# Optimization experiments

Hardware: AMD Instinct MI355X
Metric: run time of the kernel (lower is better)

## Reference

```python
import jax, jax.numpy as jnp
import numpy as np

B, NE, NR, D1, D2, L = 64, 40000, 500, 200, 200, 64
BN_EPS = 1e-5


def _batchnorm(x, gamma, beta):
    # training-mode BatchNorm1d: biased batch statistics over axis 0
    mu = jnp.mean(x, axis=0)
    var = jnp.var(x, axis=0)
    return gamma * (x - mu) * jax.lax.rsqrt(var + BN_EPS) + beta


def setup_inputs() -> dict:
    key = jax.random.key(0)
    ks = jax.random.split(key, 10)
    return {
        "e1_idx": jax.random.randint(ks[0], (B,), 0, NE),
        "r_idx": jax.random.randint(ks[1], (B,), 0, NR),
        "E": jax.random.normal(ks[2], (NE, D1), dtype=jnp.float32),
        "R": jax.random.normal(ks[3], (NR, D2), dtype=jnp.float32),
        # W ~ Uniform(-1, 1) as in the torch module
        "W": jax.random.uniform(ks[4], (D2, D1, D1), dtype=jnp.float32, minval=-1.0, maxval=1.0),
        # literals normalized into [0, 1]
        "lits": jax.random.uniform(ks[5], (NE, L), dtype=jnp.float32),
        "c": jax.random.normal(ks[6], (L,), dtype=jnp.float32) * 0.1,
        # variance buffer must be positive
        "var_l": jax.random.uniform(ks[7], (L,), dtype=jnp.float32, minval=0.5, maxval=1.5),
        "nf": jax.random.normal(ks[8], (NR, L), dtype=jnp.float32) * 0.1,
        "bn0_gamma": jnp.ones((D1,), jnp.float32),
        "bn0_beta": jnp.zeros((D1,), jnp.float32),
        "bn1_gamma": jnp.ones((D1,), jnp.float32),
        "bn1_beta": jnp.zeros((D1,), jnp.float32),
    }


def reference(e1_idx, r_idx, E, R, W, lits, c, var_l, nf,
              bn0_gamma, bn0_beta, bn1_gamma, bn1_beta):
    # --- TuckER core ---
    e1 = E[e1_idx]                                   # (B, d1)
    x = _batchnorm(e1, bn0_gamma, bn0_beta)          # (B, d1)
    r = R[r_idx]                                     # (B, d2)
    W_mat = jnp.einsum('bk,kij->bij', r, W)          # (B, d1, d1)
    x = jnp.einsum('bi,bij->bj', x, W_mat)           # (B, d1)
    x = _batchnorm(x, bn1_gamma, bn1_beta)
    score_l = x @ E.T                                # (B, N)

    # --- KBLN numeric-literal branch ---
    n_h = lits[e1_idx]                               # (B, L)
    # broadcast instead of .repeat: (B, 1, L) - (1, N, L) -> (B, N, L)
    n = n_h[:, None, :] - lits[None, :, :]
    phi = jnp.exp(-jnp.square(n - c) / var_l)        # (B, N, L)
    w_nf = nf[r_idx]                                 # (B, L)
    score_n = jnp.einsum('bnl,bl->bn', phi, w_nf)    # (B, N)

    return jax.nn.sigmoid(score_l + score_n)
```

## Files before the change

### kernel.cpp

```cpp
#include <hip/hip_runtime.h>
#include <math.h>

#define BB    64
#define NEC   40000
#define NRC   500
#define D1C   200
#define D2C   200
#define LLC   64
#define BN_EPS 1e-5f
#define LOG2E 1.4426950408889634f

#define WS_XT    0
#define WS_RT    12800
#define WS_TAP   25600
#define WS_WP    29696
#define WS_SL    33792
#define WS_X2BH  33856
#define WS_X2BL  42048
#define WS_Y     50240

typedef short s8v __attribute__((ext_vector_type(8)));
typedef float f4v __attribute__((ext_vector_type(4)));

__device__ __forceinline__ unsigned short bf16_rne(float x) {
  unsigned b = __float_as_uint(x);
  unsigned r = b + 0x7FFFu + ((b >> 16) & 1u);
  return (unsigned short)(r >> 16);
}
__device__ __forceinline__ void split2(float x, unsigned short& h,
                                       unsigned short& l) {
  h = bf16_rne(x);
  float hf = __uint_as_float(((unsigned)h) << 16);
  l = bf16_rne(x - hf);
}

typedef __attribute__((address_space(1))) const void gvoid_t;
typedef __attribute__((address_space(3))) void lvoid_t;
__device__ __forceinline__ void gload_lds16(const float* g, float* l) {
  __builtin_amdgcn_global_load_lds((gvoid_t*)g, (lvoid_t*)l, 16, 0, 0);
}

__global__ __launch_bounds__(256) void prep_kernel(
    const int* __restrict__ e1_idx, const int* __restrict__ r_idx,
    const float* __restrict__ E, const float* __restrict__ R,
    const float* __restrict__ lits, const float* __restrict__ c,
    const float* __restrict__ var_l, const float* __restrict__ nf,
    const float* __restrict__ bn0g, const float* __restrict__ bn0b,
    float* __restrict__ ws) {
  float* xT  = ws + WS_XT;
  float* rT  = ws + WS_RT;
  float* taP = ws + WS_TAP;
  float* wP  = ws + WS_WP;
  float* sl  = ws + WS_SL;
  int tid = threadIdx.x;

  if (blockIdx.x == 0) {
    if (tid < D1C) {
      int j = tid;
      float sum = 0.f, sq = 0.f;
      for (int b = 0; b < BB; b++) {
        float e = E[e1_idx[b] * D1C + j];
        sum += e; sq += e * e;
      }
      float mean = sum * (1.f / 64.f);
      float var  = sq  * (1.f / 64.f) - mean * mean;
      float inv  = __builtin_amdgcn_rsqf(var + BN_EPS);
      float g    = bn0g[j] * inv;
      float be   = bn0b[j] - mean * g;
      for (int b = 0; b < BB; b++) {
        xT[j * 64 + b] = g * E[e1_idx[b] * D1C + j] + be;
      }
    }
  } else if (blockIdx.x == 1) {
    for (int idx = tid; idx < D2C * 64; idx += 256) {
      int k = idx >> 6, b = idx & 63;
      rT[idx] = R[r_idx[b] * D2C + k];
    }
  } else if (blockIdx.x == 2) {
    for (int idx = tid; idx < LLC * 64; idx += 256) {
      int l = idx >> 6, b = idx & 63;
      float s = sqrtf(LOG2E / var_l[l]);
      float a = (lits[e1_idx[b] * LLC + l] - c[l]) * s;
      int bp = (b & 15) * 4 + (b >> 4);
      taP[l * 64 + bp] = a + a;
      wP[l * 64 + bp]  = nf[r_idx[b] * LLC + l] * __builtin_amdgcn_exp2f(-a * a);
    }
    if (tid < LLC) sl[tid] = sqrtf(LOG2E / var_l[tid]);
  } else {
    unsigned* z = (unsigned*)(ws + WS_X2BH);
    for (int i = tid; i < 16384; i += 256) z[i] = 0u;
  }
}

#define S1_STAGE(buf_, s_) do {                                         \
    int gbase_ = kbase + (s_) * 8000;                                   \
    _Pragma("unroll")                                                   \
    for (int r_ = 0; r_ < 4; r_++) {                                    \
      int off_ = r_ * 2048 + w * 256;                                   \
      int gi_ = gbase_ + off_ + lane4;                                  \
      gi_ = gi_ < 7999996 ? gi_ : 7999996;                              \
      gload_lds16(W + gi_, &Wb[buf_][off_]);                            \
    }                                                                   \
  } while (0)

__global__ __launch_bounds__(512) void stage1_kernel(
    const float* __restrict__ W, const float* __restrict__ ws_in,
    float* __restrict__ y) {
  const float* xT = ws_in + WS_XT;
  const float* rT = ws_in + WS_RT;
  __shared__ float Wb[2][8192];

  int k = blockIdx.x;
  int tid = threadIdx.x;
  int lane = tid & 63;
  int w = __builtin_amdgcn_readfirstlane(tid >> 6);
  int jc = w & 3, bh = w >> 2;
  int j4 = lane & 15, bq = lane >> 4;
  int j0 = jc * 64 + j4 * 4;
  int b0 = bh * 32 + bq * 8;
  bool jok = j0 < 200;
  int joff = jok ? j0 : 0;
  int kbase = k * 40000;
  int lane4 = lane * 4;

  float acc[4][8];
#pragma unroll
  for (int jj = 0; jj < 4; jj++)
#pragma unroll
    for (int bb = 0; bb < 8; bb++) acc[jj][bb] = 0.f;

  S1_STAGE(0, 0);
  for (int s = 0; s < 5; s++) {
    __syncthreads();
    if (s < 4) S1_STAGE((s + 1) & 1, s + 1);
    const float* Ws = Wb[s & 1];
    const float* xrow = xT + s * 40 * 64 + b0;
#pragma unroll 4
    for (int ri = 0; ri < 40; ri++) {
      float4 wv  = *(const float4*)(Ws + ri * 200 + joff);
      float4 xa  = *(const float4*)(xrow + ri * 64);
      float4 xb2 = *(const float4*)(xrow + ri * 64 + 4);
      float wc[4] = {wv.x, wv.y, wv.z, wv.w};
      float xv[8] = {xa.x, xa.y, xa.z, xa.w, xb2.x, xb2.y, xb2.z, xb2.w};
#pragma unroll
      for (int jj = 0; jj < 4; jj++)
#pragma unroll
        for (int bb = 0; bb < 8; bb++)
          acc[jj][bb] += wc[jj] * xv[bb];
    }
  }

  if (jok) {
    float4 r0 = *(const float4*)(rT + k * 64 + b0);
    float4 r1 = *(const float4*)(rT + k * 64 + b0 + 4);
    float rv[8] = {r0.x, r0.y, r0.z, r0.w, r1.x, r1.y, r1.z, r1.w};
#pragma unroll
    for (int jj = 0; jj < 4; jj++) {
      float* yo = y + (k * D1C + j0 + jj) * 64 + b0;
      float4 o0 = make_float4(acc[jj][0] * rv[0], acc[jj][1] * rv[1],
                              acc[jj][2] * rv[2], acc[jj][3] * rv[3]);
      float4 o1 = make_float4(acc[jj][4] * rv[4], acc[jj][5] * rv[5],
                              acc[jj][6] * rv[6], acc[jj][7] * rv[7]);
      *(float4*)(yo) = o0;
      *(float4*)(yo + 4) = o1;
    }
  }
}

__global__ __launch_bounds__(256) void reduce_bn1_kernel(
    const float* __restrict__ y, const float* __restrict__ bn1g,
    const float* __restrict__ bn1b, float* __restrict__ ws) {
  int j = blockIdx.x;
  int tid = threadIdx.x, b = tid & 63, kq = tid >> 6;

  float s = 0.f;
  const float* yp = y + (kq * 50 * D1C + j) * 64 + b;
#pragma unroll 10
  for (int k = 0; k < 50; k++) s += yp[k * D1C * 64];

  __shared__ float part[256];
  part[tid] = s;
  __syncthreads();
  if (tid < 64) {
    float v = part[tid] + part[64 + tid] + part[128 + tid] + part[192 + tid];
    float sum = v, sq = v * v;
#pragma unroll
    for (int o = 32; o > 0; o >>= 1) {
      sum += __shfl_xor(sum, o, 64);
      sq  += __shfl_xor(sq,  o, 64);
    }
    float mean = sum * (1.f / 64.f);
    float var  = sq  * (1.f / 64.f) - mean * mean;
    float inv  = __builtin_amdgcn_rsqf(var + BN_EPS);
    float g    = bn1g[j] * inv;
    float be   = bn1b[j] - mean * g;
    float xv   = g * v + be;
    unsigned short h, l;
    split2(xv, h, l);
    unsigned short* xh = (unsigned short*)(ws + WS_X2BH);
    unsigned short* xl = (unsigned short*)(ws + WS_X2BL);
    xh[tid * 256 + j] = h;
    xl[tid * 256 + j] = l;
  }
}

__global__ __launch_bounds__(256, 4) void final_kernel(
    const float* __restrict__ E, const float* __restrict__ lits,
    const float* __restrict__ ws, float* __restrict__ out) {
  const float* taP = ws + WS_TAP;
  const float* wP  = ws + WS_WP;
  const float* sl  = ws + WS_SL;
  const unsigned short* x2bh = (const unsigned short*)(ws + WS_X2BH);
  const unsigned short* x2bl = (const unsigned short*)(ws + WS_X2BL);

  __shared__ float SM[9216];
  unsigned short* Ah = (unsigned short*)SM;
  unsigned short* Al = Ah + 4608;
  unsigned short* Bh = Ah + 9216;
  unsigned short* Bl = Ah + 13824;

  int n0 = blockIdx.x * 64;
  int tid = threadIdx.x;
  int lane = tid & 63;
  int w = __builtin_amdgcn_readfirstlane(tid >> 6);
  int ln = lane & 15;
  int quad = lane >> 4;

  f4v acc[4];
#pragma unroll
  for (int t = 0; t < 4; t++) acc[t] = (f4v){0.f, 0.f, 0.f, 0.f};

  for (int q = 0; q < 4; q++) {
    int k0 = q * 64;
    __syncthreads();
#pragma unroll
    for (int it = 0; it < 4; it++) {
      int idx = tid + it * 256;
      int row = idx >> 4, c4 = idx & 15, cc = c4 * 4;
      float4 v = make_float4(0.f, 0.f, 0.f, 0.f);
      if (k0 + cc < 200) v = *(const float4*)(E + (n0 + row) * D1C + k0 + cc);
      unsigned short h0, l0, h1, l1, h2, l2, h3, l3;
      split2(v.x, h0, l0); split2(v.y, h1, l1);
      split2(v.z, h2, l2); split2(v.w, h3, l3);
      *(ushort4*)(Ah + row * 72 + cc) = make_ushort4(h0, h1, h2, h3);
      *(ushort4*)(Al + row * 72 + cc) = make_ushort4(l0, l1, l2, l3);
    }
#pragma unroll
    for (int it = 0; it < 4; it++) {
      int idx = tid + it * 256;
      int row = idx >> 4, c4 = idx & 15;
      *(ushort4*)(Bh + row * 72 + c4 * 4) =
          *(const ushort4*)(x2bh + row * 256 + k0 + c4 * 4);
      *(ushort4*)(Bl + row * 72 + c4 * 4) =
          *(const ushort4*)(x2bl + row * 256 + k0 + c4 * 4);
    }
    __syncthreads();

    const unsigned short* Ab  = Ah + (16 * w + ln) * 72 + quad * 8;
    const unsigned short* Alb = Al + (16 * w + ln) * 72 + quad * 8;
#pragma unroll
    for (int ks = 0; ks < 64; ks += 32) {
      s8v ah = *(const s8v*)(Ab + ks);
      s8v al = *(const s8v*)(Alb + ks);
#pragma unroll
      for (int t = 0; t < 4; t++) {
        s8v bh = *(const s8v*)(Bh + (16 * t + ln) * 72 + quad * 8 + ks);
        s8v bl = *(const s8v*)(Bl + (16 * t + ln) * 72 + quad * 8 + ks);
        acc[t] = __builtin_amdgcn_mfma_f32_16x16x32_bf16(ah, bh, acc[t], 0, 0, 0);
        acc[t] = __builtin_amdgcn_mfma_f32_16x16x32_bf16(al, bh, acc[t], 0, 0, 0);
        acc[t] = __builtin_amdgcn_mfma_f32_16x16x32_bf16(ah, bl, acc[t], 0, 0, 0);
      }
    }
  }

  float* Llds = SM;
  float* TAl  = SM + 4352;
  float* Wl   = SM + 6400;
  int nlb = 16 * w + 4 * quad;

  __syncthreads();
#pragma unroll
  for (int it = 0; it < 4; it++) {
    int idx = tid + it * 256;
    int row = idx >> 4, c4 = idx & 15;
    float4 v = *(const float4*)(lits + (n0 + row) * LLC + c4 * 4);
    int l = c4 * 4;
    Llds[(l + 0) * 68 + row] = v.x * sl[l + 0];
    Llds[(l + 1) * 68 + row] = v.y * sl[l + 1];
    Llds[(l + 2) * 68 + row] = v.z * sl[l + 2];
    Llds[(l + 3) * 68 + row] = v.w * sl[l + 3];
  }

  for (int h = 0; h < 2; h++) {
    __syncthreads();
#pragma unroll
    for (int it = 0; it < 2; it++) {
      int idx = tid + it * 256;
      ((float4*)TAl)[idx] = ((const float4*)(taP + h * 2048))[idx];
      ((float4*)Wl)[idx]  = ((const float4*)(wP  + h * 2048))[idx];
    }
    __syncthreads();
    for (int ll = 0; ll < 32; ll++) {
      float4 Lv = *(const float4*)(Llds + (h * 32 + ll) * 68 + nlb);
      float4 ta = *(const float4*)(TAl + ll * 64 + 4 * ln);
      float4 wv = *(const float4*)(Wl  + ll * 64 + 4 * ln);
      float Lc[4]  = {Lv.x, Lv.y, Lv.z, Lv.w};
      float tac[4] = {ta.x, ta.y, ta.z, ta.w};
      float wvc[4] = {wv.x, wv.y, wv.z, wv.w};
      float n2[4];
#pragma unroll
      for (int r = 0; r < 4; r++) n2[r] = -Lc[r] * Lc[r];
#pragma unroll
      for (int t = 0; t < 4; t++) {
#pragma unroll
        for (int r = 0; r < 4; r++) {
          acc[t][r] += wvc[t] *
              __builtin_amdgcn_exp2f(__builtin_fmaf(tac[t], Lc[r], n2[r]));
        }
      }
    }
  }

#pragma unroll
  for (int t = 0; t < 4; t++) {
    float4 o;
    o.x = __builtin_amdgcn_rcpf(1.f + __builtin_amdgcn_exp2f(-LOG2E * acc[t][0]));
    o.y = __builtin_amdgcn_rcpf(1.f + __builtin_amdgcn_exp2f(-LOG2E * acc[t][1]));
    o.z = __builtin_amdgcn_rcpf(1.f + __builtin_amdgcn_exp2f(-LOG2E * acc[t][2]));
    o.w = __builtin_amdgcn_rcpf(1.f + __builtin_amdgcn_exp2f(-LOG2E * acc[t][3]));
    *(float4*)(out + (size_t)(16 * t + ln) * NEC + n0 + nlb) = o;
  }
}

extern "C" void kernel_launch(void* const* d_in, const int* in_sizes, int n_in,
                              void* d_out, int out_size, void* d_ws, size_t ws_size,
                              hipStream_t stream) {
  (void)in_sizes; (void)n_in; (void)out_size; (void)ws_size;
  const int*   e1    = (const int*)d_in[0];
  const int*   ri    = (const int*)d_in[1];
  const float* E     = (const float*)d_in[2];
  const float* R     = (const float*)d_in[3];
  const float* W     = (const float*)d_in[4];
  const float* lits  = (const float*)d_in[5];
  const float* c     = (const float*)d_in[6];
  const float* var_l = (const float*)d_in[7];
  const float* nf    = (const float*)d_in[8];
  const float* bn0g  = (const float*)d_in[9];
  const float* bn0b  = (const float*)d_in[10];
  const float* bn1g  = (const float*)d_in[11];
  const float* bn1b  = (const float*)d_in[12];
  float* out = (float*)d_out;
  float* ws  = (float*)d_ws;
  float* y   = ws + WS_Y;

  prep_kernel<<<4, 256, 0, stream>>>(e1, ri, E, R, lits, c, var_l, nf,
                                     bn0g, bn0b, ws);
  stage1_kernel<<<200, 512, 0, stream>>>(W, ws, y);
  reduce_bn1_kernel<<<200, 256, 0, stream>>>(y, bn1g, bn1b, ws);
  final_kernel<<<625, 256, 0, stream>>>(E, lits, ws, out);
}
```

Measured before the change: 202.9 us.

## Split final kernel into MFMA score kernel and literal-branch kernel

The fused final kernel is split in two. One kernel computes the TuckER matmul scores with MFMA and writes the raw logits to the output. A second kernel, launched on a 2D grid that splits the batch rows in half, reads those logits back, adds the exp-heavy literal score, and applies the sigmoid. The aim is more parallelism and less register pressure for the exp-bound part, at the cost of an extra round trip of the 64x40000 output through memory and one more launch.

```diff
diff --git a/kernel.cpp b/kernel.cpp
--- a/kernel.cpp
+++ b/kernel.cpp
@@ -204,12 +204,9 @@
   }
 }
 
-__global__ __launch_bounds__(256, 4) void final_kernel(
-    const float* __restrict__ E, const float* __restrict__ lits,
-    const float* __restrict__ ws, float* __restrict__ out) {
-  const float* taP = ws + WS_TAP;
-  const float* wP  = ws + WS_WP;
-  const float* sl  = ws + WS_SL;
+__global__ __launch_bounds__(256) void final_l_kernel(
+    const float* __restrict__ E, const float* __restrict__ ws,
+    float* __restrict__ out) {
   const unsigned short* x2bh = (const unsigned short*)(ws + WS_X2BH);
   const unsigned short* x2bl = (const unsigned short*)(ws + WS_X2BL);
 
@@ -273,12 +270,31 @@
     }
   }
 
-  float* Llds = SM;
-  float* TAl  = SM + 4352;
-  float* Wl   = SM + 6400;
   int nlb = 16 * w + 4 * quad;
-
-  __syncthreads();
+#pragma unroll
+  for (int t = 0; t < 4; t++) {
+    *(f4v*)(out + (size_t)(16 * t + ln) * NEC + n0 + nlb) = acc[t];
+  }
+}
+
+__global__ __launch_bounds__(256) void final_n_kernel(
+    const float* __restrict__ lits, const float* __restrict__ ws,
+    float* __restrict__ out) {
+  const float* taP = ws + WS_TAP;
+  const float* wP  = ws + WS_WP;
+  const float* sl  = ws + WS_SL;
+
+  __shared__ float Llds[64 * 68];
+
+  int n0 = blockIdx.x * 64;
+  int yb = blockIdx.y;
+  int tid = threadIdx.x;
+  int lane = tid & 63;
+  int w = __builtin_amdgcn_readfirstlane(tid >> 6);
+  int ln = lane & 15;
+  int quad = lane >> 4;
+  int nlb = 16 * w + 4 * quad;
+
 #pragma unroll
   for (int it = 0; it < 4; it++) {
     int idx = tid + it * 256;
@@ -291,43 +307,44 @@
     Llds[(l + 3) * 68 + row] = v.w * sl[l + 3];
   }
 
-  for (int h = 0; h < 2; h++) {
-    __syncthreads();
-#pragma unroll
-    for (int it = 0; it < 2; it++) {
-      int idx = tid + it * 256;
-      ((float4*)TAl)[idx] = ((const float4*)(taP + h * 2048))[idx];
-      ((float4*)Wl)[idx]  = ((const float4*)(wP  + h * 2048))[idx];
-    }
-    __syncthreads();
-    for (int ll = 0; ll < 32; ll++) {
-      float4 Lv = *(const float4*)(Llds + (h * 32 + ll) * 68 + nlb);
-      float4 ta = *(const float4*)(TAl + ll * 64 + 4 * ln);
-      float4 wv = *(const float4*)(Wl  + ll * 64 + 4 * ln);
-      float Lc[4]  = {Lv.x, Lv.y, Lv.z, Lv.w};
-      float tac[4] = {ta.x, ta.y, ta.z, ta.w};
-      float wvc[4] = {wv.x, wv.y, wv.z, wv.w};
-      float n2[4];
-#pragma unroll
-      for (int r = 0; r < 4; r++) n2[r] = -Lc[r] * Lc[r];
-#pragma unroll
-      for (int t = 0; t < 4; t++) {
-#pragma unroll
-        for (int r = 0; r < 4; r++) {
-          acc[t][r] += wvc[t] *
-              __builtin_amdgcn_exp2f(__builtin_fmaf(tac[t], Lc[r], n2[r]));
-        }
+  f4v acc[2];
+#pragma unroll
+  for (int tt = 0; tt < 2; tt++) {
+    int t = 2 * yb + tt;
+    acc[tt] = *(const f4v*)(out + (size_t)(16 * t + ln) * NEC + n0 + nlb);
+  }
+  __syncthreads();
+
+  int tw = 4 * ln + 2 * yb;
+#pragma unroll 2
+  for (int ll = 0; ll < 64; ll++) {
+    float4 Lv = *(const float4*)(&Llds[ll * 68 + nlb]);
+    float2 ta = *(const float2*)(taP + ll * 64 + tw);
+    float2 wv = *(const float2*)(wP  + ll * 64 + tw);
+    float Lc[4]  = {Lv.x, Lv.y, Lv.z, Lv.w};
+    float tac[2] = {ta.x, ta.y};
+    float wvc[2] = {wv.x, wv.y};
+    float n2[4];
+#pragma unroll
+    for (int r = 0; r < 4; r++) n2[r] = -Lc[r] * Lc[r];
+#pragma unroll
+    for (int tt = 0; tt < 2; tt++) {
+#pragma unroll
+      for (int r = 0; r < 4; r++) {
+        acc[tt][r] += wvc[tt] *
+            __builtin_amdgcn_exp2f(__builtin_fmaf(tac[tt], Lc[r], n2[r]));
       }
     }
   }
 
 #pragma unroll
-  for (int t = 0; t < 4; t++) {
+  for (int tt = 0; tt < 2; tt++) {
+    int t = 2 * yb + tt;
     float4 o;
-    o.x = __builtin_amdgcn_rcpf(1.f + __builtin_amdgcn_exp2f(-LOG2E * acc[t][0]));
-    o.y = __builtin_amdgcn_rcpf(1.f + __builtin_amdgcn_exp2f(-LOG2E * acc[t][1]));
-    o.z = __builtin_amdgcn_rcpf(1.f + __builtin_amdgcn_exp2f(-LOG2E * acc[t][2]));
-    o.w = __builtin_amdgcn_rcpf(1.f + __builtin_amdgcn_exp2f(-LOG2E * acc[t][3]));
+    o.x = __builtin_amdgcn_rcpf(1.f + __builtin_amdgcn_exp2f(-LOG2E * acc[tt][0]));
+    o.y = __builtin_amdgcn_rcpf(1.f + __builtin_amdgcn_exp2f(-LOG2E * acc[tt][1]));
+    o.z = __builtin_amdgcn_rcpf(1.f + __builtin_amdgcn_exp2f(-LOG2E * acc[tt][2]));
+    o.w = __builtin_amdgcn_rcpf(1.f + __builtin_amdgcn_exp2f(-LOG2E * acc[tt][3]));
     *(float4*)(out + (size_t)(16 * t + ln) * NEC + n0 + nlb) = o;
   }
 }
@@ -357,5 +374,6 @@
                                      bn0g, bn0b, ws);
   stage1_kernel<<<200, 512, 0, stream>>>(W, ws, y);
   reduce_bn1_kernel<<<200, 256, 0, stream>>>(y, bn1g, bn1b, ws);
-  final_kernel<<<625, 256, 0, stream>>>(E, lits, ws, out);
-}
+  final_l_kernel<<<625, 256, 0, stream>>>(E, ws, out);
+  final_n_kernel<<<dim3(625, 2), 256, 0, stream>>>(lits, ws, out);
+}
```

Result: slower. 210.6 us (+3.8%).

## Read W directly from global in stage1 and cache gathered embeddings in prep

Applied to the files above, without the earlier changes.

Stage1 no longer double-buffers W slices through LDS with async global-to-LDS loads and barriers. Each thread now reads its float4 of W straight from global memory across all 200 rows and relies on cache reuse across the wave. This removes LDS traffic and __syncthreads, but gives up explicit prefetch and latency hiding for a bandwidth-heavy 32 MB read. Separately, the BN0 prep keeps the 64 gathered E values in registers instead of reloading them.

```diff
diff --git a/kernel.cpp b/kernel.cpp
--- a/kernel.cpp
+++ b/kernel.cpp
@@ -32,12 +32,6 @@
   h = bf16_rne(x);
   float hf = __uint_as_float(((unsigned)h) << 16);
   l = bf16_rne(x - hf);
-}
-
-typedef __attribute__((address_space(1))) const void gvoid_t;
-typedef __attribute__((address_space(3))) void lvoid_t;
-__device__ __forceinline__ void gload_lds16(const float* g, float* l) {
-  __builtin_amdgcn_global_load_lds((gvoid_t*)g, (lvoid_t*)l, 16, 0, 0);
 }
 
 __global__ __launch_bounds__(256) void prep_kernel(
@@ -57,9 +51,12 @@
   if (blockIdx.x == 0) {
     if (tid < D1C) {
       int j = tid;
+      float ev[64];
       float sum = 0.f, sq = 0.f;
+#pragma unroll
       for (int b = 0; b < BB; b++) {
         float e = E[e1_idx[b] * D1C + j];
+        ev[b] = e;
         sum += e; sq += e * e;
       }
       float mean = sum * (1.f / 64.f);
@@ -67,8 +64,9 @@
       float inv  = __builtin_amdgcn_rsqf(var + BN_EPS);
       float g    = bn0g[j] * inv;
       float be   = bn0b[j] - mean * g;
+#pragma unroll
       for (int b = 0; b < BB; b++) {
-        xT[j * 64 + b] = g * E[e1_idx[b] * D1C + j] + be;
+        xT[j * 64 + b] = g * ev[b] + be;
       }
     }
   } else if (blockIdx.x == 1) {
@@ -92,23 +90,11 @@
   }
 }
 
-#define S1_STAGE(buf_, s_) do {                                         \
-    int gbase_ = kbase + (s_) * 8000;                                   \
-    _Pragma("unroll")                                                   \
-    for (int r_ = 0; r_ < 4; r_++) {                                    \
-      int off_ = r_ * 2048 + w * 256;                                   \
-      int gi_ = gbase_ + off_ + lane4;                                  \
-      gi_ = gi_ < 7999996 ? gi_ : 7999996;                              \
-      gload_lds16(W + gi_, &Wb[buf_][off_]);                            \
-    }                                                                   \
-  } while (0)
-
 __global__ __launch_bounds__(512) void stage1_kernel(
     const float* __restrict__ W, const float* __restrict__ ws_in,
     float* __restrict__ y) {
   const float* xT = ws_in + WS_XT;
   const float* rT = ws_in + WS_RT;
-  __shared__ float Wb[2][8192];
 
   int k = blockIdx.x;
   int tid = threadIdx.x;
@@ -120,8 +106,8 @@
   int b0 = bh * 32 + bq * 8;
   bool jok = j0 < 200;
   int joff = jok ? j0 : 0;
-  int kbase = k * 40000;
-  int lane4 = lane * 4;
+  const float* Wk = W + k * 40000 + joff;
+  const float* xp = xT + b0;
 
   float acc[4][8];
 #pragma unroll
@@ -129,25 +115,18 @@
 #pragma unroll
     for (int bb = 0; bb < 8; bb++) acc[jj][bb] = 0.f;
 
-  S1_STAGE(0, 0);
-  for (int s = 0; s < 5; s++) {
-    __syncthreads();
-    if (s < 4) S1_STAGE((s + 1) & 1, s + 1);
-    const float* Ws = Wb[s & 1];
-    const float* xrow = xT + s * 40 * 64 + b0;
 #pragma unroll 4
-    for (int ri = 0; ri < 40; ri++) {
-      float4 wv  = *(const float4*)(Ws + ri * 200 + joff);
-      float4 xa  = *(const float4*)(xrow + ri * 64);
-      float4 xb2 = *(const float4*)(xrow + ri * 64 + 4);
-      float wc[4] = {wv.x, wv.y, wv.z, wv.w};
-      float xv[8] = {xa.x, xa.y, xa.z, xa.w, xb2.x, xb2.y, xb2.z, xb2.w};
-#pragma unroll
-      for (int jj = 0; jj < 4; jj++)
-#pragma unroll
-        for (int bb = 0; bb < 8; bb++)
-          acc[jj][bb] += wc[jj] * xv[bb];
-    }
+  for (int i = 0; i < D1C; i++) {
+    float4 wv  = *(const float4*)(Wk + i * 200);
+    float4 xa  = *(const float4*)(xp + i * 64);
+    float4 xb2 = *(const float4*)(xp + i * 64 + 4);
+    float wc[4] = {wv.x, wv.y, wv.z, wv.w};
+    float xv[8] = {xa.x, xa.y, xa.z, xa.w, xb2.x, xb2.y, xb2.z, xb2.w};
+#pragma unroll
+    for (int jj = 0; jj < 4; jj++)
+#pragma unroll
+      for (int bb = 0; bb < 8; bb++)
+        acc[jj][bb] += wc[jj] * xv[bb];
   }
 
   if (jok) {
```

Measured after the change: 213.2 us. 1.05x slower.
